# Kernel optimization log

Measured on AMD Instinct MI355X. Metric: run time of the kernel, lower is better.

Reference implementation:

```python
import jax, jax.numpy as jnp
import numpy as np

NUM_STEPS = 32
HIDDEN = 1024
BATCH = 1024


def setup_inputs() -> dict:
    key = jax.random.key(0)
    ks = jax.random.split(key, 10)
    s = 1.0 / np.sqrt(HIDDEN)  # PyTorch LSTM/Linear init scale
    return {
        "in_data": jax.random.normal(ks[0], (BATCH, 1), dtype=jnp.float32),
        "batch_size": BATCH,
        "h0": jax.random.normal(ks[1], (1, BATCH, HIDDEN), dtype=jnp.float32),
        "c0": jax.random.normal(ks[2], (1, BATCH, HIDDEN), dtype=jnp.float32),
        # LSTM params (PyTorch layout: gates stacked [i, f, g, o])
        "W_ih": jax.random.uniform(ks[3], (4 * HIDDEN, 1), jnp.float32, -s, s),
        "W_hh": jax.random.uniform(ks[4], (4 * HIDDEN, HIDDEN), jnp.float32, -s, s),
        "b_ih": jax.random.uniform(ks[5], (4 * HIDDEN,), jnp.float32, -s, s),
        "b_hh": jax.random.uniform(ks[6], (4 * HIDDEN,), jnp.float32, -s, s),
        # output Linear(hidden_dim, 1)
        "W_out": jax.random.uniform(ks[7], (1, HIDDEN), jnp.float32, -s, s),
        "b_out": jax.random.uniform(ks[8], (1,), jnp.float32, -s, s),
    }


def reference(in_data, batch_size, h0, c0, W_ih, W_hh, b_ih, b_hh, W_out, b_out):
    # (seq_len=1) then Linear(H->1); the scalar output feeds back as next input.
    h = h0[0]  # (B, H)
    c = c0[0]  # (B, H)
    bias = b_ih + b_hh

    def step(carry, _):
        x, h, c = carry  # x: (B, 1)
        gates = x @ W_ih.T + h @ W_hh.T + bias  # (B, 4H)
        i, f, g, o = jnp.split(gates, 4, axis=-1)
        c_new = jax.nn.sigmoid(f) * c + jax.nn.sigmoid(i) * jnp.tanh(g)
        h_new = jax.nn.sigmoid(o) * jnp.tanh(c_new)
        y = h_new @ W_out.T + b_out  # (B, 1)
        return (y, h_new, c_new), y[:, 0]

    _, ys = jax.lax.scan(step, (in_data, h, c), None, length=NUM_STEPS)
    # ys: (num_steps, B) -> (B, num_steps), matching stack().squeeze(2).permute(1,0)
    return ys.T
```

## Files before the change

### kernel.cpp

```cpp
#include <hip/hip_runtime.h>

#define H 1024
#define FH 4096
#define T 32

typedef unsigned short u16;
typedef unsigned int u32;
typedef __attribute__((ext_vector_type(8))) short short8;
typedef __attribute__((ext_vector_type(4))) u32 u32x4;
typedef __attribute__((ext_vector_type(4))) float f32x4;

#define HSZ (1u << 20)

__device__ __forceinline__ u16 f2b(float f) {
    union { float f; u32 i; } x; x.f = f;
    u32 r = x.i + 0x7fff + ((x.i >> 16) & 1);
    return (u16)(r >> 16);
}
__device__ __forceinline__ float b2f(u16 u) {
    union { u32 i; float f; } x; x.i = ((u32)u) << 16; return x.f;
}
__device__ __forceinline__ float sigm(float x) { return 1.f / (1.f + __expf(-x)); }

__global__ void prep_weff_k(const float* __restrict__ Whh, const float* __restrict__ Wih,
                            const float* __restrict__ Wo, u16* __restrict__ weff) {
    int idx = (blockIdx.x * 256 + threadIdx.x) * 8;
    int r = idx >> 10, k = idx & 1023;
    float wih = Wih[r];
    short8 outv;
#pragma unroll
    for (int e = 0; e < 8; e++) {
        float v = Whh[idx + e] + wih * Wo[k + e];
        outv[e] = (short)f2b(v);
    }
    *(short8*)(weff + idx) = outv;
}

__global__ void prep_misc_k(const float* __restrict__ h0, const float* __restrict__ bih,
                            const float* __restrict__ bhh, const float* __restrict__ bo,
                            const float* __restrict__ Wih,
                            u16* __restrict__ hbase, float* __restrict__ biasp,
                            float* __restrict__ out) {
    int i = (blockIdx.x * 256 + threadIdx.x) * 4;
#pragma unroll
    for (int e = 0; e < 4; e++) hbase[i + e] = f2b(h0[i + e]);
    if (blockIdx.x == 0) {
        for (int b = threadIdx.x; b < FH; b += 256)
            biasp[b] = bih[b] + bhh[b] + bo[0] * Wih[b];
    }
    if (blockIdx.x < 32) {
        float b0 = bo[0];
        int o = blockIdx.x * 1024 + threadIdx.x * 4;
#pragma unroll
        for (int e = 0; e < 4; e++) out[o + e] = b0;
    }
}

__global__ void prep_d0_k(const float* __restrict__ in_data, const float* __restrict__ h0,
                          const float* __restrict__ Wo, const float* __restrict__ bo,
                          float* __restrict__ dd0) {
    int lane = threadIdx.x & 63, wid = threadIdx.x >> 6;
    for (int rr = 0; rr < 4; ++rr) {
        int m = blockIdx.x * 16 + (wid << 2) + rr;
        const float* hp = h0 + ((u32)m << 10) + lane * 16;
        const float* wp = Wo + lane * 16;
        float s = 0.f;
#pragma unroll
        for (int e = 0; e < 16; e++) s += hp[e] * wp[e];
#pragma unroll
        for (int off = 32; off >= 1; off >>= 1) s += __shfl_xor(s, off, 64);
        if (lane == 0) dd0[m] = in_data[m] - s - bo[0];
    }
}

template<bool COH>
__global__ __launch_bounds__(512) void lstm_persist_k(
    const u16* __restrict__ weff, u16* __restrict__ hbase,
    const float* __restrict__ biasp, const float* __restrict__ dd0,
    const float* __restrict__ Wih, const float* __restrict__ Wo,
    const float* __restrict__ c0, float* __restrict__ out, u32* __restrict__ cnt)
{
    __shared__ __align__(16) char smem[65536];
    float* gb = (float*)smem;

    const int tid = threadIdx.x;
    const int lane = tid & 63, wid = tid >> 6;
    const int wr = wid >> 2, wc = wid & 3;
    const int bx = blockIdx.x;
    const int mb = (bx >> 3) & 7;
    const int jb = (bx & 7) * 4 + (bx >> 6);
    const int m0 = mb << 7, j0 = jb << 5;
    const int rl = lane & 15, sl = lane >> 4;
    const int jj = tid & 31, grp = tid >> 5;
    const int j = j0 + jj;

    const float bs0 = biasp[j], bs1 = biasp[H + j], bs2 = biasp[2 * H + j], bs3 = biasp[3 * H + j];
    const float wi0 = Wih[j], wi1 = Wih[H + j], wi2 = Wih[2 * H + j], wi3 = Wih[3 * H + j];
    const float woj = Wo[j];
    float c_reg[8];
#pragma unroll
    for (int p = 0; p < 2; ++p)
#pragma unroll
        for (int q = 0; q < 4; ++q)
            c_reg[p * 4 + q] = c0[(u32)(m0 + p * 64 + grp * 4 + q) * H + j];

    int crow[4], csub[4], wrow_[4];
#pragma unroll
    for (int i = 0; i < 4; i++) {
        int c_ = tid + i * 512;
        crow[i] = c_ >> 4; csub[i] = c_ & 15;
        wrow_[i] = ((crow[i] >> 5) << 10) + j0 + (crow[i] & 31);
    }

    for (int s = 0; s < T; ++s) {
        const u16* hin = hbase + (u32)(COH ? (s & 1) : s) * HSZ;
        u16* hout      = hbase + (u32)(COH ? ((s + 1) & 1) : (s + 1)) * HSZ;

        f32x4 acc[4][2];
#pragma unroll
        for (int im = 0; im < 4; im++)
#pragma unroll
            for (int in_ = 0; in_ < 2; in_++) acc[im][in_] = (f32x4){0.f, 0.f, 0.f, 0.f};

        u32x4 ph[4], pw[4];
        auto loadt = [&](int kk) {
#pragma unroll
            for (int i = 0; i < 4; i++) {
                const u16* pa = hin + ((u32)(m0 + crow[i]) << 10) + kk + csub[i] * 8;
                if constexpr (COH) {
                    asm volatile("global_load_dwordx4 %0, %1, off sc0 sc1"
                                 : "=v"(ph[i]) : "v"(pa));
                } else {
                    ph[i] = *(const u32x4*)pa;
                }
                pw[i] = *(const u32x4*)(weff + ((u32)wrow_[i] << 10) + kk + csub[i] * 8);
            }
        };
        auto writet = [&]() {
            if constexpr (COH) {
                asm volatile("s_waitcnt vmcnt(0)" ::: "memory");
                __builtin_amdgcn_sched_barrier(0);
            }
#pragma unroll
            for (int i = 0; i < 4; i++) {
                int sb = (crow[i] * 256 + csub[i] * 16) ^ ((crow[i] & 15) << 4);
                *(u32x4*)(smem + sb) = ph[i];
                *(u32x4*)(smem + 32768 + sb) = pw[i];
            }
        };

        loadt(0); writet();

        for (int it = 0; it < 8; ++it) {
            __syncthreads();
            if (it < 7) loadt((it + 1) * 128);
#pragma unroll
            for (int ks = 0; ks < 4; ++ks) {
                short8 af[4], bg[2];
#pragma unroll
                for (int im = 0; im < 4; ++im) {
                    int row = (wr << 6) + (im << 4) + rl;
                    int sb = (row * 256 + (ks * 4 + sl) * 16) ^ ((row & 15) << 4);
                    af[im] = *(const short8*)(smem + sb);
                }
#pragma unroll
                for (int in_ = 0; in_ < 2; ++in_) {
                    int row = (wc << 5) + (in_ << 4) + rl;
                    int sb = (row * 256 + (ks * 4 + sl) * 16) ^ ((row & 15) << 4);
                    bg[in_] = *(const short8*)(smem + 32768 + sb);
                }
#pragma unroll
                for (int im = 0; im < 4; ++im)
#pragma unroll
                    for (int in_ = 0; in_ < 2; ++in_)
                        acc[im][in_] = __builtin_amdgcn_mfma_f32_16x16x32_bf16(
                            af[im], bg[in_], acc[im][in_], 0, 0, 0);
            }
            __syncthreads();
            if (it < 7) writet();
        }

#pragma unroll
        for (int p = 0; p < 2; ++p) {
            __syncthreads();
            if (wr == p) {
#pragma unroll
                for (int im = 0; im < 4; ++im)
#pragma unroll
                    for (int in_ = 0; in_ < 2; ++in_)
#pragma unroll
                        for (int q = 0; q < 4; ++q)
                            gb[(im * 16 + sl * 4 + q) * 132 + (wc << 5) + (in_ << 4) + rl]
                                = acc[im][in_][q];
            }
            __syncthreads();
#pragma unroll
            for (int q = 0; q < 4; ++q) {
                int m_loc = grp * 4 + q;
                int m_abs = m0 + p * 64 + m_loc;
                const float* gr = gb + m_loc * 132;
                float gi  = gr[jj] + bs0;
                float gf_ = gr[32 + jj] + bs1;
                float gg_ = gr[64 + jj] + bs2;
                float go_ = gr[96 + jj] + bs3;
                if (s == 0) {
                    float d = dd0[m_abs];
                    gi += d * wi0; gf_ += d * wi1; gg_ += d * wi2; go_ += d * wi3;
                }
                float cv = c_reg[p * 4 + q];
                float cn = sigm(gf_) * cv + sigm(gi) * tanhf(gg_);
                float hn = sigm(go_) * tanhf(cn);
                c_reg[p * 4 + q] = cn;

                u32 hv = (u32)f2b(hn);
                u32 nb = __shfl_down(hv, 1, 32);
                if ((jj & 1) == 0) {
                    u32* hp = (u32*)(hout + (((u32)m_abs << 10) + j));
                    __hip_atomic_store(hp, (nb << 16) | hv,
                                       __ATOMIC_RELAXED, __HIP_MEMORY_SCOPE_AGENT);
                }

                float yp = hn * woj;
                yp += __shfl_xor(yp, 16, 32);
                yp += __shfl_xor(yp, 8, 32);
                yp += __shfl_xor(yp, 4, 32);
                yp += __shfl_xor(yp, 2, 32);
                yp += __shfl_xor(yp, 1, 32);
                if (jj == 0)
                    __hip_atomic_fetch_add(out + (u32)m_abs * T + s, yp,
                                           __ATOMIC_RELAXED, __HIP_MEMORY_SCOPE_AGENT);
            }
        }

        if (s < T - 1) {
            __syncthreads();
            if (tid == 0) {
                u32* cc = cnt + ((u32)(s * 8 + mb) << 4);
                __hip_atomic_fetch_add(cc, 1u, __ATOMIC_RELAXED, __HIP_MEMORY_SCOPE_AGENT);
                while (__hip_atomic_load(cc, __ATOMIC_RELAXED, __HIP_MEMORY_SCOPE_AGENT) < 32u)
                    __builtin_amdgcn_s_sleep(2);
            }
            __syncthreads();
        }
    }
}

extern "C" void kernel_launch(void* const* d_in, const int* in_sizes, int n_in,
                              void* d_out, int out_size, void* d_ws, size_t ws_size,
                              hipStream_t stream) {
    const float* in_data = (const float*)d_in[0];
    const float* h0  = (const float*)d_in[2];
    const float* c0  = (const float*)d_in[3];
    const float* Wih = (const float*)d_in[4];
    const float* Whh = (const float*)d_in[5];
    const float* bih = (const float*)d_in[6];
    const float* bhh = (const float*)d_in[7];
    const float* Wo  = (const float*)d_in[8];
    const float* bo  = (const float*)d_in[9];
    float* out = (float*)d_out;
    char* ws = (char*)d_ws;

    u16*   weff  = (u16*)ws;
    float* biasp = (float*)(ws + (8u << 20));
    float* dd0   = (float*)(ws + (8u << 20) + 16384);
    u32*   cnt   = (u32*)(ws + (8u << 20) + 32768);
    u16*   hbase = (u16*)(ws + (8u << 20) + 65536);

    bool rot = ws_size >= ((size_t)76 << 20);

    hipMemsetAsync(cnt, 0, 32 * 8 * 16 * sizeof(u32), stream);
    hipLaunchKernelGGL(prep_weff_k, dim3(2048), dim3(256), 0, stream, Whh, Wih, Wo, weff);
    hipLaunchKernelGGL(prep_misc_k, dim3(1024), dim3(256), 0, stream,
                       h0, bih, bhh, bo, Wih, hbase, biasp, out);
    hipLaunchKernelGGL(prep_d0_k, dim3(64), dim3(256), 0, stream, in_data, h0, Wo, bo, dd0);

    if (rot)
        hipLaunchKernelGGL((lstm_persist_k<false>), dim3(256), dim3(512), 0, stream,
                           weff, hbase, biasp, dd0, Wih, Wo, c0, out, cnt);
    else
        hipLaunchKernelGGL((lstm_persist_k<true>), dim3(256), dim3(512), 0, stream,
                           weff, hbase, biasp, dd0, Wih, Wo, c0, out, cnt);
}
```

Measured before the change: 535.1 us.

## Pre-swizzle weights and hidden state into MFMA fragment layout and keep weights in registers

Weights and hidden state are rewritten into a fragment-native layout so each lane loads its MFMA operands directly. B fragments come straight from global memory into registers, and h tiles are staged into LDS via global_load_lds. The kernel switches to 32x32x16 MFMAs with 64-row by 64-column tiles and a 16-way per-row-block barrier, and uses fast tanh and sigmoid approximations. This removes the LDS staging of weights and the swizzled LDS reads, at the cost of more global weight traffic per step and a different synchronization grouping.

```diff
diff --git a/kernel.cpp b/kernel.cpp
--- a/kernel.cpp
+++ b/kernel.cpp
@@ -3,47 +3,57 @@
 #define H 1024
 #define FH 4096
 #define T 32
+#define HSZ (1u << 20)
 
 typedef unsigned short u16;
 typedef unsigned int u32;
 typedef __attribute__((ext_vector_type(8))) short short8;
+typedef __attribute__((ext_vector_type(16))) float f32x16;
 typedef __attribute__((ext_vector_type(4))) u32 u32x4;
-typedef __attribute__((ext_vector_type(4))) float f32x4;
-
-#define HSZ (1u << 20)
 
 __device__ __forceinline__ u16 f2b(float f) {
     union { float f; u32 i; } x; x.f = f;
     u32 r = x.i + 0x7fff + ((x.i >> 16) & 1);
     return (u16)(r >> 16);
 }
-__device__ __forceinline__ float b2f(u16 u) {
-    union { u32 i; float f; } x; x.i = ((u32)u) << 16; return x.f;
-}
-__device__ __forceinline__ float sigm(float x) { return 1.f / (1.f + __expf(-x)); }
+__device__ __forceinline__ float sigm(float x) {
+    return __fdividef(1.f, 1.f + __expf(-x));
+}
+__device__ __forceinline__ float ftanh(float x) {
+    float t = __expf(-2.f * fabsf(x));
+    return copysignf(__fdividef(1.f - t, 1.f + t), x);
+}
 
 __global__ void prep_weff_k(const float* __restrict__ Whh, const float* __restrict__ Wih,
-                            const float* __restrict__ Wo, u16* __restrict__ weff) {
-    int idx = (blockIdx.x * 256 + threadIdx.x) * 8;
-    int r = idx >> 10, k = idx & 1023;
-    float wih = Wih[r];
-    short8 outv;
-#pragma unroll
-    for (int e = 0; e < 8; e++) {
-        float v = Whh[idx + e] + wih * Wo[k + e];
-        outv[e] = (short)f2b(v);
-    }
-    *(short8*)(weff + idx) = outv;
+                            const float* __restrict__ Wo, u16* __restrict__ wf) {
+    int t = blockIdx.x * 256 + threadIdx.x;
+    int frag = t >> 6, l = t & 63;
+    int ct = frag >> 6, kf = frag & 63;
+    int row = ct * 32 + (l & 31);
+    int k0 = kf * 16 + (l >> 5) * 8;
+    float wih = Wih[row];
+    const float* wr_ = Whh + (u32)row * H + k0;
+    const float* wo_ = Wo + k0;
+    short8 v;
+#pragma unroll
+    for (int e = 0; e < 8; e++) v[e] = (short)f2b(wr_[e] + wih * wo_[e]);
+    *(short8*)(wf + ((u32)frag << 9) + l * 8) = v;
 }
 
 __global__ void prep_misc_k(const float* __restrict__ h0, const float* __restrict__ bih,
                             const float* __restrict__ bhh, const float* __restrict__ bo,
-                            const float* __restrict__ Wih,
-                            u16* __restrict__ hbase, float* __restrict__ biasp,
-                            float* __restrict__ out) {
-    int i = (blockIdx.x * 256 + threadIdx.x) * 4;
-#pragma unroll
-    for (int e = 0; e < 4; e++) hbase[i + e] = f2b(h0[i + e]);
+                            const float* __restrict__ Wih, u16* __restrict__ hb0,
+                            float* __restrict__ biasp, float* __restrict__ out) {
+    int t = blockIdx.x * 256 + threadIdx.x;
+    int r = t >> 7, k0 = (t & 127) * 8;
+    int mb = r >> 6, rl_ = r & 63;
+    int rt = rl_ >> 5, kf = k0 >> 4, lhi = (k0 >> 3) & 1;
+    int ln = (rl_ & 31) + lhi * 32;
+    const float* src = h0 + (u32)r * H + k0;
+    short8 v;
+#pragma unroll
+    for (int e = 0; e < 8; e++) v[e] = (short)f2b(src[e]);
+    *(short8*)(hb0 + (u32)mb * 65536 + (u32)((kf * 2 + rt) << 9) + ln * 8) = v;
     if (blockIdx.x == 0) {
         for (int b = threadIdx.x; b < FH; b += 256)
             biasp[b] = bih[b] + bhh[b] + bo[0] * Wih[b];
@@ -87,157 +97,142 @@
     const int lane = tid & 63, wid = tid >> 6;
     const int wr = wid >> 2, wc = wid & 3;
     const int bx = blockIdx.x;
-    const int mb = (bx >> 3) & 7;
-    const int jb = (bx & 7) * 4 + (bx >> 6);
-    const int m0 = mb << 7, j0 = jb << 5;
-    const int rl = lane & 15, sl = lane >> 4;
-    const int jj = tid & 31, grp = tid >> 5;
-    const int j = j0 + jj;
-
-    const float bs0 = biasp[j], bs1 = biasp[H + j], bs2 = biasp[2 * H + j], bs3 = biasp[3 * H + j];
-    const float wi0 = Wih[j], wi1 = Wih[H + j], wi2 = Wih[2 * H + j], wi3 = Wih[3 * H + j];
+    const int mb = (bx >> 3) & 15;
+    const int jb = (bx & 7) * 2 + (bx >> 7);
+    const int m0 = mb << 6;
+    const int jj = lane, rgrp = wid;
+    const int j = (jb << 6) + jj;
+
+    const float bs0 = biasp[j], bs1 = biasp[H + j], bs2 = biasp[2*H + j], bs3 = biasp[3*H + j];
+    const float wi0 = Wih[j], wi1 = Wih[H + j], wi2 = Wih[2*H + j], wi3 = Wih[3*H + j];
     const float woj = Wo[j];
     float c_reg[8];
 #pragma unroll
-    for (int p = 0; p < 2; ++p)
-#pragma unroll
-        for (int q = 0; q < 4; ++q)
-            c_reg[p * 4 + q] = c0[(u32)(m0 + p * 64 + grp * 4 + q) * H + j];
-
-    int crow[4], csub[4], wrow_[4];
-#pragma unroll
-    for (int i = 0; i < 4; i++) {
-        int c_ = tid + i * 512;
-        crow[i] = c_ >> 4; csub[i] = c_ & 15;
-        wrow_[i] = ((crow[i] >> 5) << 10) + j0 + (crow[i] & 31);
-    }
+    for (int q = 0; q < 8; ++q)
+        c_reg[q] = c0[(u32)(m0 + rgrp * 8 + q) * H + j];
+
+    const u16* wB = weff + (((u32)(wc * 32 + jb * 2) * 64) << 9) + lane * 8;
+
+    u32x4 ph[2];
 
     for (int s = 0; s < T; ++s) {
-        const u16* hin = hbase + (u32)(COH ? (s & 1) : s) * HSZ;
-        u16* hout      = hbase + (u32)(COH ? ((s + 1) & 1) : (s + 1)) * HSZ;
-
-        f32x4 acc[4][2];
-#pragma unroll
-        for (int im = 0; im < 4; im++)
-#pragma unroll
-            for (int in_ = 0; in_ < 2; in_++) acc[im][in_] = (f32x4){0.f, 0.f, 0.f, 0.f};
-
-        u32x4 ph[4], pw[4];
-        auto loadt = [&](int kk) {
-#pragma unroll
-            for (int i = 0; i < 4; i++) {
-                const u16* pa = hin + ((u32)(m0 + crow[i]) << 10) + kk + csub[i] * 8;
+        const u16* hreg = hbase + (u32)(COH ? (s & 1) : s) * HSZ + (u32)mb * 65536;
+        u16* hwreg      = hbase + (u32)(COH ? ((s + 1) & 1) : (s + 1)) * HSZ + (u32)mb * 65536;
+
+        f32x16 acc0, acc1;
+#pragma unroll
+        for (int e = 0; e < 16; e++) { acc0[e] = 0.f; acc1[e] = 0.f; }
+
+        auto stage_issue = [&](int b, int it) {
+#pragma unroll
+            for (int i = 0; i < 2; ++i) {
+                const u16* src = hreg + ((u32)((it * 8 + wid) * 2 + i) << 9) + lane * 8;
                 if constexpr (COH) {
                     asm volatile("global_load_dwordx4 %0, %1, off sc0 sc1"
-                                 : "=v"(ph[i]) : "v"(pa));
+                                 : "=v"(ph[i]) : "v"(src));
                 } else {
-                    ph[i] = *(const u32x4*)pa;
-                }
-                pw[i] = *(const u32x4*)(weff + ((u32)wrow_[i] << 10) + kk + csub[i] * 8);
+                    __builtin_amdgcn_global_load_lds(
+                        (const u32*)src,
+                        (u32*)(smem + b * 16384 + (wid * 2 + i) * 1024),
+                        16, 0, 0);
+                }
             }
         };
-        auto writet = [&]() {
-            if constexpr (COH) {
-                asm volatile("s_waitcnt vmcnt(0)" ::: "memory");
-                __builtin_amdgcn_sched_barrier(0);
-            }
-#pragma unroll
-            for (int i = 0; i < 4; i++) {
-                int sb = (crow[i] * 256 + csub[i] * 16) ^ ((crow[i] & 15) << 4);
-                *(u32x4*)(smem + sb) = ph[i];
-                *(u32x4*)(smem + 32768 + sb) = pw[i];
-            }
+        auto stage_write = [&](int b) {
+            asm volatile("s_waitcnt vmcnt(0)" ::: "memory");
+            __builtin_amdgcn_sched_barrier(0);
+#pragma unroll
+            for (int i = 0; i < 2; ++i)
+                *(u32x4*)(smem + b * 16384 + (wid * 2 + i) * 1024 + lane * 16) = ph[i];
         };
 
-        loadt(0); writet();
+        stage_issue(0, 0);
+        if constexpr (COH) stage_write(0);
 
         for (int it = 0; it < 8; ++it) {
-            __syncthreads();
-            if (it < 7) loadt((it + 1) * 128);
-#pragma unroll
-            for (int ks = 0; ks < 4; ++ks) {
-                short8 af[4], bg[2];
-#pragma unroll
-                for (int im = 0; im < 4; ++im) {
-                    int row = (wr << 6) + (im << 4) + rl;
-                    int sb = (row * 256 + (ks * 4 + sl) * 16) ^ ((row & 15) << 4);
-                    af[im] = *(const short8*)(smem + sb);
-                }
-#pragma unroll
-                for (int in_ = 0; in_ < 2; ++in_) {
-                    int row = (wc << 5) + (in_ << 4) + rl;
-                    int sb = (row * 256 + (ks * 4 + sl) * 16) ^ ((row & 15) << 4);
-                    bg[in_] = *(const short8*)(smem + 32768 + sb);
-                }
-#pragma unroll
-                for (int im = 0; im < 4; ++im)
-#pragma unroll
-                    for (int in_ = 0; in_ < 2; ++in_)
-                        acc[im][in_] = __builtin_amdgcn_mfma_f32_16x16x32_bf16(
-                            af[im], bg[in_], acc[im][in_], 0, 0, 0);
-            }
-            __syncthreads();
-            if (it < 7) writet();
+            const int b = it & 1;
+            __syncthreads();
+            short8 b0[8], b1[8];
+            const u16* wB0 = wB + (u32)it * 4096;
+#pragma unroll
+            for (int kf = 0; kf < 8; ++kf) b0[kf] = *(const short8*)(wB0 + kf * 512);
+#pragma unroll
+            for (int kf = 0; kf < 8; ++kf) b1[kf] = *(const short8*)(wB0 + 32768 + kf * 512);
+            if (it < 7) stage_issue(b ^ 1, it + 1);
+            const char* abase = smem + b * 16384 + wr * 1024;
+#pragma unroll
+            for (int kf = 0; kf < 8; ++kf) {
+                short8 a = *(const short8*)(abase + kf * 2048 + lane * 16);
+                acc0 = __builtin_amdgcn_mfma_f32_32x32x16_bf16(a, b0[kf], acc0, 0, 0, 0);
+                acc1 = __builtin_amdgcn_mfma_f32_32x32x16_bf16(a, b1[kf], acc1, 0, 0, 0);
+            }
+            if constexpr (COH) { if (it < 7) stage_write(b ^ 1); }
         }
 
+        float gi[8], gf_[8];
+        const int crb = 4 * (lane >> 5);
+        const int ccol = lane & 31;
 #pragma unroll
         for (int p = 0; p < 2; ++p) {
             __syncthreads();
-            if (wr == p) {
-#pragma unroll
-                for (int im = 0; im < 4; ++im)
-#pragma unroll
-                    for (int in_ = 0; in_ < 2; ++in_)
-#pragma unroll
-                        for (int q = 0; q < 4; ++q)
-                            gb[(im * 16 + sl * 4 + q) * 132 + (wc << 5) + (in_ << 4) + rl]
-                                = acc[im][in_][q];
-            }
-            __syncthreads();
-#pragma unroll
-            for (int q = 0; q < 4; ++q) {
-                int m_loc = grp * 4 + q;
-                int m_abs = m0 + p * 64 + m_loc;
-                const float* gr = gb + m_loc * 132;
-                float gi  = gr[jj] + bs0;
-                float gf_ = gr[32 + jj] + bs1;
-                float gg_ = gr[64 + jj] + bs2;
-                float go_ = gr[96 + jj] + bs3;
-                if (s == 0) {
-                    float d = dd0[m_abs];
-                    gi += d * wi0; gf_ += d * wi1; gg_ += d * wi2; go_ += d * wi3;
-                }
-                float cv = c_reg[p * 4 + q];
-                float cn = sigm(gf_) * cv + sigm(gi) * tanhf(gg_);
-                float hn = sigm(go_) * tanhf(cn);
-                c_reg[p * 4 + q] = cn;
-
-                u32 hv = (u32)f2b(hn);
-                u32 nb = __shfl_down(hv, 1, 32);
-                if ((jj & 1) == 0) {
-                    u32* hp = (u32*)(hout + (((u32)m_abs << 10) + j));
-                    __hip_atomic_store(hp, (nb << 16) | hv,
-                                       __ATOMIC_RELAXED, __HIP_MEMORY_SCOPE_AGENT);
-                }
-
-                float yp = hn * woj;
-                yp += __shfl_xor(yp, 16, 32);
-                yp += __shfl_xor(yp, 8, 32);
-                yp += __shfl_xor(yp, 4, 32);
-                yp += __shfl_xor(yp, 2, 32);
-                yp += __shfl_xor(yp, 1, 32);
-                if (jj == 0)
-                    __hip_atomic_fetch_add(out + (u32)m_abs * T + s, yp,
-                                           __ATOMIC_RELAXED, __HIP_MEMORY_SCOPE_AGENT);
+            if ((wc >> 1) == p) {
+                const int cb = (wc & 1) * 64;
+#pragma unroll
+                for (int reg = 0; reg < 16; ++reg) {
+                    int rowl = wr * 32 + (reg & 3) + 8 * (reg >> 2) + crb;
+                    gb[rowl * 132 + cb + ccol]      = acc0[reg];
+                    gb[rowl * 132 + cb + 32 + ccol] = acc1[reg];
+                }
+            }
+            __syncthreads();
+            if (p == 0) {
+#pragma unroll
+                for (int q = 0; q < 8; ++q) {
+                    int rloc = rgrp * 8 + q;
+                    gi[q]  = gb[rloc * 132 + jj] + bs0;
+                    gf_[q] = gb[rloc * 132 + 64 + jj] + bs1;
+                }
+            } else {
+#pragma unroll
+                for (int q = 0; q < 8; ++q) {
+                    int rloc = rgrp * 8 + q;
+                    int m_abs = m0 + rloc;
+                    float gg_ = gb[rloc * 132 + jj] + bs2;
+                    float go_ = gb[rloc * 132 + 64 + jj] + bs3;
+                    float giq = gi[q], gfq = gf_[q];
+                    if (s == 0) {
+                        float d = dd0[m_abs];
+                        giq += d * wi0; gfq += d * wi1; gg_ += d * wi2; go_ += d * wi3;
+                    }
+                    float cn = sigm(gfq) * c_reg[q] + sigm(giq) * ftanh(gg_);
+                    float hn = sigm(go_) * ftanh(cn);
+                    c_reg[q] = cn;
+                    if (s < T - 1) {
+                        u32 hv = (u32)f2b(hn);
+                        u32 nb = __shfl_down(hv, 1);
+                        if (!(jj & 1)) {
+                            u32 idx = ((u32)((j >> 4) * 2 + (rloc >> 5)) << 9)
+                                      + ((rloc & 31) + ((j >> 3) & 1) * 32) * 8 + (j & 7);
+                            __hip_atomic_store((u32*)(hwreg + idx), (nb << 16) | hv,
+                                               __ATOMIC_RELAXED, __HIP_MEMORY_SCOPE_AGENT);
+                        }
+                    }
+                    float yp = hn * woj;
+#pragma unroll
+                    for (int off = 32; off >= 1; off >>= 1) yp += __shfl_xor(yp, off);
+                    if (jj == 0)
+                        __hip_atomic_fetch_add(out + (u32)m_abs * T + s, yp,
+                                               __ATOMIC_RELAXED, __HIP_MEMORY_SCOPE_AGENT);
+                }
             }
         }
 
         if (s < T - 1) {
             __syncthreads();
             if (tid == 0) {
-                u32* cc = cnt + ((u32)(s * 8 + mb) << 4);
+                u32* cc = cnt + ((u32)(s * 16 + mb) << 4);
                 __hip_atomic_fetch_add(cc, 1u, __ATOMIC_RELAXED, __HIP_MEMORY_SCOPE_AGENT);
-                while (__hip_atomic_load(cc, __ATOMIC_RELAXED, __HIP_MEMORY_SCOPE_AGENT) < 32u)
+                while (__hip_atomic_load(cc, __ATOMIC_RELAXED, __HIP_MEMORY_SCOPE_AGENT) < 16u)
                     __builtin_amdgcn_s_sleep(2);
             }
             __syncthreads();
@@ -263,14 +258,14 @@
     u16*   weff  = (u16*)ws;
     float* biasp = (float*)(ws + (8u << 20));
     float* dd0   = (float*)(ws + (8u << 20) + 16384);
-    u32*   cnt   = (u32*)(ws + (8u << 20) + 32768);
+    u32*   cnt   = (u32*)(ws + (8u << 20) + 24576);
     u16*   hbase = (u16*)(ws + (8u << 20) + 65536);
 
     bool rot = ws_size >= ((size_t)76 << 20);
 
-    hipMemsetAsync(cnt, 0, 32 * 8 * 16 * sizeof(u32), stream);
+    hipMemsetAsync(cnt, 0, 32768, stream);
     hipLaunchKernelGGL(prep_weff_k, dim3(2048), dim3(256), 0, stream, Whh, Wih, Wo, weff);
-    hipLaunchKernelGGL(prep_misc_k, dim3(1024), dim3(256), 0, stream,
+    hipLaunchKernelGGL(prep_misc_k, dim3(512), dim3(256), 0, stream,
                        h0, bih, bhh, bo, Wih, hbase, biasp, out);
     hipLaunchKernelGGL(prep_d0_k, dim3(64), dim3(256), 0, stream, in_data, h0, Wo, bo, dd0);
 
```

After: 1.607 ms. 200% more time.

## Double-buffer LDS with direct global-to-LDS loads and split-K waves

Applied to the files above, without the earlier changes.

Restructures the persistent LSTM GEMM loop to double-buffer LDS (128 KB), using global_load_lds direct-to-LDS copies on the non-coherent path so the next K-tile streams in while MFMAs run, dropping one barrier per iteration. Waves are reorganised into a 2-way K split with 64x64 per-wave tiles, and the partial sums are reduced through two LDS gate buffers. It also raises wave priority during MFMA, swaps tanhf for an exp-based fast tanh, and skips the hidden-state store on the final step. The risks are lower occupancy from the larger LDS footprint, an extra reduction pass, and slightly different numerics from the fast tanh.

```diff
diff --git a/kernel.cpp b/kernel.cpp
--- a/kernel.cpp
+++ b/kernel.cpp
@@ -3,24 +3,26 @@
 #define H 1024
 #define FH 4096
 #define T 32
+#define HSZ (1u << 20)
 
 typedef unsigned short u16;
 typedef unsigned int u32;
 typedef __attribute__((ext_vector_type(8))) short short8;
+typedef __attribute__((ext_vector_type(4))) float f32x4;
 typedef __attribute__((ext_vector_type(4))) u32 u32x4;
-typedef __attribute__((ext_vector_type(4))) float f32x4;
-
-#define HSZ (1u << 20)
 
 __device__ __forceinline__ u16 f2b(float f) {
     union { float f; u32 i; } x; x.f = f;
     u32 r = x.i + 0x7fff + ((x.i >> 16) & 1);
     return (u16)(r >> 16);
 }
-__device__ __forceinline__ float b2f(u16 u) {
-    union { u32 i; float f; } x; x.i = ((u32)u) << 16; return x.f;
-}
-__device__ __forceinline__ float sigm(float x) { return 1.f / (1.f + __expf(-x)); }
+__device__ __forceinline__ float sigm(float x) {
+    return __fdividef(1.f, 1.f + __expf(-x));
+}
+__device__ __forceinline__ float ftanh(float x) {
+    float t = __expf(-2.f * fabsf(x));
+    return copysignf(__fdividef(1.f - t, 1.f + t), x);
+}
 
 __global__ void prep_weff_k(const float* __restrict__ Whh, const float* __restrict__ Wih,
                             const float* __restrict__ Wo, u16* __restrict__ weff) {
@@ -80,146 +82,162 @@
     const float* __restrict__ Wih, const float* __restrict__ Wo,
     const float* __restrict__ c0, float* __restrict__ out, u32* __restrict__ cnt)
 {
-    __shared__ __align__(16) char smem[65536];
-    float* gb = (float*)smem;
+    __shared__ __align__(16) char smem[131072];
+    float* gb0 = (float*)smem;
+    float* gb1 = (float*)(smem + 65536);
 
     const int tid = threadIdx.x;
     const int lane = tid & 63, wid = tid >> 6;
-    const int wr = wid >> 2, wc = wid & 3;
+    const int kg = wid >> 2;
+    const int wrr = (wid >> 1) & 1, wcc = wid & 1;
     const int bx = blockIdx.x;
     const int mb = (bx >> 3) & 7;
     const int jb = (bx & 7) * 4 + (bx >> 6);
     const int m0 = mb << 7, j0 = jb << 5;
     const int rl = lane & 15, sl = lane >> 4;
-    const int jj = tid & 31, grp = tid >> 5;
+    const int jj = tid & 31, rgrp = tid >> 5;
     const int j = j0 + jj;
 
-    const float bs0 = biasp[j], bs1 = biasp[H + j], bs2 = biasp[2 * H + j], bs3 = biasp[3 * H + j];
-    const float wi0 = Wih[j], wi1 = Wih[H + j], wi2 = Wih[2 * H + j], wi3 = Wih[3 * H + j];
+    const float bs0 = biasp[j], bs1 = biasp[H + j], bs2 = biasp[2*H + j], bs3 = biasp[3*H + j];
+    const float wi0 = Wih[j], wi1 = Wih[H + j], wi2 = Wih[2*H + j], wi3 = Wih[3*H + j];
     const float woj = Wo[j];
     float c_reg[8];
 #pragma unroll
     for (int p = 0; p < 2; ++p)
 #pragma unroll
         for (int q = 0; q < 4; ++q)
-            c_reg[p * 4 + q] = c0[(u32)(m0 + p * 64 + grp * 4 + q) * H + j];
-
-    int crow[4], csub[4], wrow_[4];
+            c_reg[p * 4 + q] = c0[(u32)(m0 + p * 64 + rgrp * 4 + q) * H + j];
+
+    int arow[4], brow[4], koff[4], dstA[4], dstB[4];
 #pragma unroll
     for (int i = 0; i < 4; i++) {
         int c_ = tid + i * 512;
-        crow[i] = c_ >> 4; csub[i] = c_ & 15;
-        wrow_[i] = ((crow[i] >> 5) << 10) + j0 + (crow[i] & 31);
+        int row = c_ >> 4, cs = c_ & 15;
+        int cs_src = COH ? cs : (cs ^ (row & 15));
+        koff[i] = (cs_src >> 3) * 512 + (cs_src & 7) * 8;
+        arow[i] = m0 + row;
+        brow[i] = ((row >> 5) << 10) + j0 + (row & 31);
+        int dchunk = COH ? (row * 16 + (cs ^ (row & 15))) : c_;
+        dstA[i] = dchunk * 16;
+        dstB[i] = 32768 + dchunk * 16;
     }
 
     for (int s = 0; s < T; ++s) {
         const u16* hin = hbase + (u32)(COH ? (s & 1) : s) * HSZ;
         u16* hout      = hbase + (u32)(COH ? ((s + 1) & 1) : (s + 1)) * HSZ;
 
-        f32x4 acc[4][2];
+        f32x4 acc[4][4];
 #pragma unroll
         for (int im = 0; im < 4; im++)
 #pragma unroll
-            for (int in_ = 0; in_ < 2; in_++) acc[im][in_] = (f32x4){0.f, 0.f, 0.f, 0.f};
+            for (int in_ = 0; in_ < 4; in_++) acc[im][in_] = (f32x4){0.f, 0.f, 0.f, 0.f};
 
         u32x4 ph[4], pw[4];
-        auto loadt = [&](int kk) {
+        auto issue = [&](int buf, int it) {
 #pragma unroll
             for (int i = 0; i < 4; i++) {
-                const u16* pa = hin + ((u32)(m0 + crow[i]) << 10) + kk + csub[i] * 8;
+                const u16* pa = hin + ((u32)arow[i] << 10) + it * 64 + koff[i];
+                const u16* pb = weff + ((u32)brow[i] << 10) + it * 64 + koff[i];
                 if constexpr (COH) {
                     asm volatile("global_load_dwordx4 %0, %1, off sc0 sc1"
                                  : "=v"(ph[i]) : "v"(pa));
+                    pw[i] = *(const u32x4*)pb;
                 } else {
-                    ph[i] = *(const u32x4*)pa;
-                }
-                pw[i] = *(const u32x4*)(weff + ((u32)wrow_[i] << 10) + kk + csub[i] * 8);
+                    __builtin_amdgcn_global_load_lds((const u32*)pa,
+                        (u32*)(smem + buf * 65536 + dstA[i]), 16, 0, 0);
+                    __builtin_amdgcn_global_load_lds((const u32*)pb,
+                        (u32*)(smem + buf * 65536 + dstB[i]), 16, 0, 0);
+                }
             }
         };
-        auto writet = [&]() {
-            if constexpr (COH) {
-                asm volatile("s_waitcnt vmcnt(0)" ::: "memory");
-                __builtin_amdgcn_sched_barrier(0);
-            }
+        auto cwrite = [&](int buf) {
+            asm volatile("s_waitcnt vmcnt(0)" ::: "memory");
+            __builtin_amdgcn_sched_barrier(0);
 #pragma unroll
             for (int i = 0; i < 4; i++) {
-                int sb = (crow[i] * 256 + csub[i] * 16) ^ ((crow[i] & 15) << 4);
-                *(u32x4*)(smem + sb) = ph[i];
-                *(u32x4*)(smem + 32768 + sb) = pw[i];
+                *(u32x4*)(smem + buf * 65536 + dstA[i]) = ph[i];
+                *(u32x4*)(smem + buf * 65536 + dstB[i]) = pw[i];
             }
         };
 
-        loadt(0); writet();
+        issue(0, 0);
+        if constexpr (COH) cwrite(0);
 
         for (int it = 0; it < 8; ++it) {
-            __syncthreads();
-            if (it < 7) loadt((it + 1) * 128);
-#pragma unroll
-            for (int ks = 0; ks < 4; ++ks) {
-                short8 af[4], bg[2];
+            const int buf = it & 1;
+            __syncthreads();
+            if (it < 7) issue(buf ^ 1, it + 1);
+            const char* base = smem + buf * 65536;
+            __builtin_amdgcn_s_setprio(1);
+#pragma unroll
+            for (int ks = 0; ks < 2; ++ks) {
+                short8 af[4], bg[4];
 #pragma unroll
                 for (int im = 0; im < 4; ++im) {
-                    int row = (wr << 6) + (im << 4) + rl;
-                    int sb = (row * 256 + (ks * 4 + sl) * 16) ^ ((row & 15) << 4);
-                    af[im] = *(const short8*)(smem + sb);
-                }
-#pragma unroll
-                for (int in_ = 0; in_ < 2; ++in_) {
-                    int row = (wc << 5) + (in_ << 4) + rl;
-                    int sb = (row * 256 + (ks * 4 + sl) * 16) ^ ((row & 15) << 4);
-                    bg[in_] = *(const short8*)(smem + 32768 + sb);
+                    int row = wrr * 64 + im * 16 + rl;
+                    int sb = row * 256 + (((kg * 8 + ks * 4 + sl) * 16) ^ ((row & 15) << 4));
+                    af[im] = *(const short8*)(base + sb);
+                }
+#pragma unroll
+                for (int in_ = 0; in_ < 4; ++in_) {
+                    int n = wcc * 64 + in_ * 16 + rl;
+                    int sb = 32768 + n * 256 + (((kg * 8 + ks * 4 + sl) * 16) ^ ((n & 15) << 4));
+                    bg[in_] = *(const short8*)(base + sb);
                 }
 #pragma unroll
                 for (int im = 0; im < 4; ++im)
 #pragma unroll
-                    for (int in_ = 0; in_ < 2; ++in_)
+                    for (int in_ = 0; in_ < 4; ++in_)
                         acc[im][in_] = __builtin_amdgcn_mfma_f32_16x16x32_bf16(
                             af[im], bg[in_], acc[im][in_], 0, 0, 0);
             }
-            __syncthreads();
-            if (it < 7) writet();
+            __builtin_amdgcn_s_setprio(0);
+            if constexpr (COH) { if (it < 7) cwrite(buf ^ 1); }
         }
 
 #pragma unroll
         for (int p = 0; p < 2; ++p) {
             __syncthreads();
-            if (wr == p) {
+            if (wrr == p) {
+                float* g = kg ? gb1 : gb0;
 #pragma unroll
                 for (int im = 0; im < 4; ++im)
 #pragma unroll
-                    for (int in_ = 0; in_ < 2; ++in_)
-#pragma unroll
-                        for (int q = 0; q < 4; ++q)
-                            gb[(im * 16 + sl * 4 + q) * 132 + (wc << 5) + (in_ << 4) + rl]
-                                = acc[im][in_][q];
+                    for (int in_ = 0; in_ < 4; ++in_)
+#pragma unroll
+                        for (int qq = 0; qq < 4; ++qq) {
+                            int r = im * 16 + sl * 4 + qq;
+                            g[r * 132 + wcc * 64 + in_ * 16 + rl] = acc[im][in_][qq];
+                        }
             }
             __syncthreads();
 #pragma unroll
             for (int q = 0; q < 4; ++q) {
-                int m_loc = grp * 4 + q;
-                int m_abs = m0 + p * 64 + m_loc;
-                const float* gr = gb + m_loc * 132;
-                float gi  = gr[jj] + bs0;
-                float gf_ = gr[32 + jj] + bs1;
-                float gg_ = gr[64 + jj] + bs2;
-                float go_ = gr[96 + jj] + bs3;
+                int rloc = rgrp * 4 + q;
+                int m_abs = m0 + p * 64 + rloc;
+                const float* g0 = gb0 + rloc * 132;
+                const float* g1 = gb1 + rloc * 132;
+                float gi  = g0[jj]      + g1[jj]      + bs0;
+                float gf_ = g0[32 + jj] + g1[32 + jj] + bs1;
+                float gg_ = g0[64 + jj] + g1[64 + jj] + bs2;
+                float go_ = g0[96 + jj] + g1[96 + jj] + bs3;
                 if (s == 0) {
                     float d = dd0[m_abs];
                     gi += d * wi0; gf_ += d * wi1; gg_ += d * wi2; go_ += d * wi3;
                 }
-                float cv = c_reg[p * 4 + q];
-                float cn = sigm(gf_) * cv + sigm(gi) * tanhf(gg_);
-                float hn = sigm(go_) * tanhf(cn);
+                float cn = sigm(gf_) * c_reg[p * 4 + q] + sigm(gi) * ftanh(gg_);
+                float hn = sigm(go_) * ftanh(cn);
                 c_reg[p * 4 + q] = cn;
 
-                u32 hv = (u32)f2b(hn);
-                u32 nb = __shfl_down(hv, 1, 32);
-                if ((jj & 1) == 0) {
-                    u32* hp = (u32*)(hout + (((u32)m_abs << 10) + j));
-                    __hip_atomic_store(hp, (nb << 16) | hv,
-                                       __ATOMIC_RELAXED, __HIP_MEMORY_SCOPE_AGENT);
-                }
-
+                if (s < T - 1) {
+                    u32 hv = (u32)f2b(hn);
+                    u32 nb = __shfl_down(hv, 1, 32);
+                    if (!(jj & 1)) {
+                        u32* hp = (u32*)(hout + (((u32)m_abs << 10) + j));
+                        __hip_atomic_store(hp, (nb << 16) | hv,
+                                           __ATOMIC_RELAXED, __HIP_MEMORY_SCOPE_AGENT);
+                    }
+                }
                 float yp = hn * woj;
                 yp += __shfl_xor(yp, 16, 32);
                 yp += __shfl_xor(yp, 8, 32);
@@ -263,12 +281,12 @@
     u16*   weff  = (u16*)ws;
     float* biasp = (float*)(ws + (8u << 20));
     float* dd0   = (float*)(ws + (8u << 20) + 16384);
-    u32*   cnt   = (u32*)(ws + (8u << 20) + 32768);
+    u32*   cnt   = (u32*)(ws + (8u << 20) + 24576);
     u16*   hbase = (u16*)(ws + (8u << 20) + 65536);
 
     bool rot = ws_size >= ((size_t)76 << 20);
 
-    hipMemsetAsync(cnt, 0, 32 * 8 * 16 * sizeof(u32), stream);
+    hipMemsetAsync(cnt, 0, 16384, stream);
     hipLaunchKernelGGL(prep_weff_k, dim3(2048), dim3(256), 0, stream, Whh, Wih, Wo, weff);
     hipLaunchKernelGGL(prep_misc_k, dim3(1024), dim3(256), 0, stream,
                        h0, bih, bhh, bo, Wih, hbase, biasp, out);
```

Result: slower. 672.8 us (+25.7%).
